# Optimization experiments

Hardware: AMD Instinct MI355X
Metric: run time of the kernel (lower is better)

Reference implementation:

```python
import jax, jax.numpy as jnp
import numpy as np

B, T, E = 2, 512, 1024        # batch, max_tokens, embedding dim
S, A = 2048, 30               # num_spans, max_arg_span


def setup_inputs() -> dict:
    key = jax.random.key(0)
    k1, k2, k3, k4 = jax.random.split(key, 4)
    x = jax.random.normal(k1, (B, T, E), dtype=jnp.float32)
    W = jax.random.normal(k2, (E, 1), dtype=jnp.float32) * (1.0 / np.sqrt(E))
    b = jnp.zeros((1,), dtype=jnp.float32)
    start = jax.random.randint(k3, (S,), 0, T, dtype=jnp.int32)
    width = jax.random.randint(k4, (S,), 1, A + 1, dtype=jnp.int32)
    end = jnp.minimum(start + width - 1, T - 1).astype(jnp.int32)
    return {"x": x, "W": W, "b": b, "start": start, "end": end}


def reference(x, W, b, start, end):
    # span_indices: clamp start+offset to last token, shape [S, A]
    span_idx = jnp.minimum(jnp.arange(A)[None, :] + start[:, None], T - 1)
    # gather span token embeddings: [B, S, A, E]
    span_emb = x[:, span_idx, :]
    # tiny per-token head score: Dense(1, relu) -> [B, T, 1]
    head_scores = jax.nn.relu(x @ W + b)
    # validity mask over span positions (log-mask), [S, A]
    span_width = end - start + 1
    valid = jnp.arange(A)[None, :] < span_width[:, None]
    log_mask = jnp.where(valid, 0.0, -jnp.inf)
    # gather scores per span position, add log-mask: [B, S, A, 1]
    span_head = head_scores[:, span_idx, :] + log_mask[None, :, :, None]
    # softmax over span-position axis (axis=2)
    attn = jax.nn.softmax(span_head, axis=2)
    # weighted-sum pooling over span positions -> [B, S, E]
    return jnp.sum(span_emb * attn, axis=2)
```

## Files before the change

### kernel.cpp

```cpp
#include <hip/hip_runtime.h>
#include <math.h>

#define TT 512
#define EE 1024
#define AA 30

typedef float f32x4 __attribute__((ext_vector_type(4)));

__device__ __forceinline__ unsigned bf16rne(float f) {
    unsigned u = __float_as_uint(f);
    return (u + 0x7fffu + ((u >> 16) & 1u)) >> 16;
}
__device__ __forceinline__ float blo(unsigned u) { return __uint_as_float(u << 16); }
__device__ __forceinline__ float bhi(unsigned u) { return __uint_as_float(u & 0xffff0000u); }

__global__ __launch_bounds__(256) void head_kernel(const float* __restrict__ x,
                                                   const float* __restrict__ W,
                                                   const float* __restrict__ bias,
                                                   float* __restrict__ head,
                                                   ushort* __restrict__ x16, int BT) {
    int row  = blockIdx.x * 4 + (threadIdx.x >> 6);
    int lane = threadIdx.x & 63;
    if (row >= BT) return;
    const f32x4* xr = reinterpret_cast<const f32x4*>(x + (size_t)row * EE);
    const f32x4* wr = reinterpret_cast<const f32x4*>(W);
    uint2* cr = reinterpret_cast<uint2*>(x16 + (size_t)row * EE);
    float acc = 0.f;
    #pragma unroll
    for (int k = 0; k < 4; ++k) {
        int i = lane + 64 * k;
        f32x4 xv = xr[i];
        f32x4 wv = wr[i];
        acc += xv.x * wv.x + xv.y * wv.y + xv.z * wv.z + xv.w * wv.w;
        if (x16) {
            uint2 pk;
            pk.x = bf16rne(xv.x) | (bf16rne(xv.y) << 16);
            pk.y = bf16rne(xv.z) | (bf16rne(xv.w) << 16);
            cr[i] = pk;
        }
    }
    #pragma unroll
    for (int off = 32; off; off >>= 1) acc += __shfl_xor(acc, off, 64);
    if (lane == 0) head[row] = fmaxf(acc + bias[0], 0.0f);
}

__global__ __launch_bounds__(256) void span16_kernel(const ushort* __restrict__ x16,
                                                     const float* __restrict__ head,
                                                     const int* __restrict__ start,
                                                     const int* __restrict__ end,
                                                     float* __restrict__ out, int S) {
    int p = blockIdx.x;
    __shared__ float wts[2][AA];

    int wv = threadIdx.x >> 6, l64 = threadIdx.x & 63;
    if (wv < 2) {
        int gg = 2 * p + wv;
        int bb = gg / S, ss = gg - bb * S;
        int st0 = start[ss];
        int nA0 = min(end[ss] - st0 + 1, AA);
        bool valid = l64 < nA0;
        int idx = st0 + l64; if (idx > TT - 1) idx = TT - 1;
        float sc = valid ? head[bb * TT + idx] : -INFINITY;
        float m = sc;
        #pragma unroll
        for (int off = 32; off; off >>= 1) m = fmaxf(m, __shfl_xor(m, off, 64));
        float e = valid ? __expf(sc - m) : 0.0f;
        float sum = e;
        #pragma unroll
        for (int off = 32; off; off >>= 1) sum += __shfl_xor(sum, off, 64);
        if (valid) wts[wv][l64] = e / sum;
    }
    __syncthreads();

    int sp   = threadIdx.x >> 7;
    int lane = threadIdx.x & 127;
    int gg = 2 * p + sp;
    int b = gg / S, s = gg - b * S;
    int st = start[s];
    int nA = min(end[s] - st + 1, AA);

    const uint4* xr = reinterpret_cast<const uint4*>(x16 + (size_t)b * TT * EE);
    f32x4 acc0 = (f32x4)(0.f), acc1 = (f32x4)(0.f);
    for (int a = 0; a < nA; ++a) {
        float w = wts[sp][a];
        uint4 v = xr[(size_t)(st + a) * (EE / 8) + lane];
        acc0.x += w * blo(v.x); acc0.y += w * bhi(v.x);
        acc0.z += w * blo(v.y); acc0.w += w * bhi(v.y);
        acc1.x += w * blo(v.z); acc1.y += w * bhi(v.z);
        acc1.z += w * blo(v.w); acc1.w += w * bhi(v.w);
    }
    f32x4* op = reinterpret_cast<f32x4*>(out) + (size_t)gg * (EE / 4) + 2 * lane;
    __builtin_nontemporal_store(acc0, op);
    __builtin_nontemporal_store(acc1, op + 1);
}

__global__ __launch_bounds__(256) void span_kernel(const float* __restrict__ x,
                                                   const float* __restrict__ head,
                                                   const int* __restrict__ start,
                                                   const int* __restrict__ end,
                                                   float* __restrict__ out, int S) {
    int bs = blockIdx.x;
    int b = bs / S, s = bs - b * S;
    int st = start[s];
    int nA = min(end[s] - st + 1, AA);
    __shared__ float wts[AA];
    int tid = threadIdx.x;
    if (tid < 64) {
        int a = tid;
        bool valid = (a < nA);
        int idx = st + a; if (idx > TT - 1) idx = TT - 1;
        float sc = valid ? head[b * TT + idx] : -INFINITY;
        float m = sc;
        #pragma unroll
        for (int off = 32; off; off >>= 1) m = fmaxf(m, __shfl_xor(m, off, 64));
        float e = valid ? __expf(sc - m) : 0.0f;
        float sum = e;
        #pragma unroll
        for (int off = 32; off; off >>= 1) sum += __shfl_xor(sum, off, 64);
        if (valid) wts[a] = e / sum;
    }
    __syncthreads();
    const f32x4* xb = reinterpret_cast<const f32x4*>(x + (size_t)b * TT * EE);
    f32x4 acc = (f32x4)(0.f);
    for (int a = 0; a < nA; ++a) {
        acc += wts[a] * xb[(size_t)(st + a) * (EE / 4) + tid];
    }
    f32x4* op = reinterpret_cast<f32x4*>(out) + (size_t)bs * (EE / 4) + tid;
    __builtin_nontemporal_store(acc, op);
}

extern "C" void kernel_launch(void* const* d_in, const int* in_sizes, int n_in,
                              void* d_out, int out_size, void* d_ws, size_t ws_size,
                              hipStream_t stream) {
    const float* x     = (const float*)d_in[0];
    const float* W     = (const float*)d_in[1];
    const float* bias  = (const float*)d_in[2];
    const int*   start = (const int*)d_in[3];
    const int*   end   = (const int*)d_in[4];
    float*       out   = (float*)d_out;

    const int BT = in_sizes[0] / EE;
    const int S  = in_sizes[3];
    const int B  = BT / TT;

    float*  head = (float*)d_ws;
    size_t  need = 8192 + (size_t)BT * EE * sizeof(ushort);
    ushort* x16  = (ws_size >= need) ? (ushort*)((char*)d_ws + 8192) : nullptr;

    head_kernel<<<(BT + 3) / 4, 256, 0, stream>>>(x, W, bias, head, x16, BT);
    if (x16 && (S & 1) == 0) {
        span16_kernel<<<B * S / 2, 256, 0, stream>>>(x16, head, start, end, out, S);
    } else {
        span_kernel<<<B * S, 256, 0, stream>>>(x, head, start, end, out, S);
    }
}
```

Baseline: 20.93 us.

## Counting-sort spans by start and remap blocks per XCD for L2 locality

Adds an extra block to the head kernel that counting-sorts span indices by start token into an order array. The span kernel reads spans in that sorted order and maps blocks round-robin so each group of eight consecutive block IDs covers one contiguous chunk of sorted spans. The goal is for spans with overlapping token rows to land on the same XCD and hit its L2 instead of going to HBM. It also makes the bf16 copy stores nontemporal. The costs are an extra indirection, writes to output rows in scattered order, and a serial sort block that runs alongside the head computation.

Result: no change. 21.30 us (+1.8%).

```diff
diff --git a/kernel.cpp b/kernel.cpp
--- a/kernel.cpp
+++ b/kernel.cpp
@@ -5,7 +5,8 @@
 #define EE 1024
 #define AA 30
 
-typedef float f32x4 __attribute__((ext_vector_type(4)));
+typedef float    f32x4 __attribute__((ext_vector_type(4)));
+typedef unsigned u32x2 __attribute__((ext_vector_type(2)));
 
 __device__ __forceinline__ unsigned bf16rne(float f) {
     unsigned u = __float_as_uint(f);
@@ -14,17 +15,57 @@
 __device__ __forceinline__ float blo(unsigned u) { return __uint_as_float(u << 16); }
 __device__ __forceinline__ float bhi(unsigned u) { return __uint_as_float(u & 0xffff0000u); }
 
-__global__ __launch_bounds__(256) void head_kernel(const float* __restrict__ x,
-                                                   const float* __restrict__ W,
-                                                   const float* __restrict__ bias,
-                                                   float* __restrict__ head,
-                                                   ushort* __restrict__ x16, int BT) {
-    int row  = blockIdx.x * 4 + (threadIdx.x >> 6);
-    int lane = threadIdx.x & 63;
+__global__ __launch_bounds__(256) void head_sort_kernel(const float* __restrict__ x,
+                                                        const float* __restrict__ W,
+                                                        const float* __restrict__ bias,
+                                                        const int* __restrict__ start,
+                                                        float* __restrict__ head,
+                                                        ushort* __restrict__ x16,
+                                                        int* __restrict__ order,
+                                                        int BT, int S, int HB) {
+    int tid = threadIdx.x;
+    if ((int)blockIdx.x == HB) {
+        __shared__ int cnt[TT];
+        __shared__ int wsum[4];
+        for (int i = tid; i < TT; i += 256) cnt[i] = 0;
+        __syncthreads();
+        for (int s = tid; s < S; s += 256) {
+            int k = start[s]; k = k < 0 ? 0 : (k > TT - 1 ? TT - 1 : k);
+            atomicAdd(&cnt[k], 1);
+        }
+        __syncthreads();
+        int a0 = cnt[2 * tid], a1 = cnt[2 * tid + 1];
+        int pair = a0 + a1;
+        int lane = tid & 63, wid = tid >> 6;
+        int v = pair;
+        #pragma unroll
+        for (int off = 1; off < 64; off <<= 1) {
+            int u = __shfl_up(v, off, 64);
+            if (lane >= off) v += u;
+        }
+        if (lane == 63) wsum[wid] = v;
+        __syncthreads();
+        int base = 0;
+        #pragma unroll
+        for (int w = 0; w < 4; ++w) if (w < wid) base += wsum[w];
+        int excl = base + v - pair;
+        __syncthreads();
+        cnt[2 * tid] = excl;
+        cnt[2 * tid + 1] = excl + a0;
+        __syncthreads();
+        for (int s = tid; s < S; s += 256) {
+            int k = start[s]; k = k < 0 ? 0 : (k > TT - 1 ? TT - 1 : k);
+            int pos = atomicAdd(&cnt[k], 1);
+            order[pos] = s;
+        }
+        return;
+    }
+    int row  = blockIdx.x * 4 + (tid >> 6);
+    int lane = tid & 63;
     if (row >= BT) return;
     const f32x4* xr = reinterpret_cast<const f32x4*>(x + (size_t)row * EE);
     const f32x4* wr = reinterpret_cast<const f32x4*>(W);
-    uint2* cr = reinterpret_cast<uint2*>(x16 + (size_t)row * EE);
+    u32x2* cr = reinterpret_cast<u32x2*>(x16 + (size_t)row * EE);
     float acc = 0.f;
     #pragma unroll
     for (int k = 0; k < 4; ++k) {
@@ -32,35 +73,40 @@
         f32x4 xv = xr[i];
         f32x4 wv = wr[i];
         acc += xv.x * wv.x + xv.y * wv.y + xv.z * wv.z + xv.w * wv.w;
-        if (x16) {
-            uint2 pk;
-            pk.x = bf16rne(xv.x) | (bf16rne(xv.y) << 16);
-            pk.y = bf16rne(xv.z) | (bf16rne(xv.w) << 16);
-            cr[i] = pk;
-        }
+        u32x2 pk;
+        pk.x = bf16rne(xv.x) | (bf16rne(xv.y) << 16);
+        pk.y = bf16rne(xv.z) | (bf16rne(xv.w) << 16);
+        __builtin_nontemporal_store(pk, cr + i);
     }
     #pragma unroll
     for (int off = 32; off; off >>= 1) acc += __shfl_xor(acc, off, 64);
     if (lane == 0) head[row] = fmaxf(acc + bias[0], 0.0f);
 }
 
+template <int BINNED>
 __global__ __launch_bounds__(256) void span16_kernel(const ushort* __restrict__ x16,
                                                      const float* __restrict__ head,
                                                      const int* __restrict__ start,
                                                      const int* __restrict__ end,
-                                                     float* __restrict__ out, int S) {
-    int p = blockIdx.x;
+                                                     const int* __restrict__ order,
+                                                     float* __restrict__ out, int S, int G8) {
     __shared__ float wts[2][AA];
+    __shared__ int sid[2], sbb[2];
+
+    int g0 = BINNED ? ((blockIdx.x & 7) * G8 + ((blockIdx.x >> 3) << 1))
+                    : (blockIdx.x * 2);
 
     int wv = threadIdx.x >> 6, l64 = threadIdx.x & 63;
     if (wv < 2) {
-        int gg = 2 * p + wv;
-        int bb = gg / S, ss = gg - bb * S;
-        int st0 = start[ss];
-        int nA0 = min(end[ss] - st0 + 1, AA);
-        bool valid = l64 < nA0;
-        int idx = st0 + l64; if (idx > TT - 1) idx = TT - 1;
-        float sc = valid ? head[bb * TT + idx] : -INFINITY;
+        int g = g0 + wv;
+        int b = g / S, r = g - b * S;
+        int s = BINNED ? order[r] : r;
+        if (l64 == 0) { sid[wv] = s; sbb[wv] = b; }
+        int st = start[s];
+        int nA = min(end[s] - st + 1, AA);
+        bool valid = l64 < nA;
+        int idx = st + l64; if (idx > TT - 1) idx = TT - 1;
+        float sc = valid ? head[b * TT + idx] : -INFINITY;
         float m = sc;
         #pragma unroll
         for (int off = 32; off; off >>= 1) m = fmaxf(m, __shfl_xor(m, off, 64));
@@ -74,8 +120,7 @@
 
     int sp   = threadIdx.x >> 7;
     int lane = threadIdx.x & 127;
-    int gg = 2 * p + sp;
-    int b = gg / S, s = gg - b * S;
+    int s = sid[sp], b = sbb[sp];
     int st = start[s];
     int nA = min(end[s] - st + 1, AA);
 
@@ -89,7 +134,7 @@
         acc1.x += w * blo(v.z); acc1.y += w * bhi(v.z);
         acc1.z += w * blo(v.w); acc1.w += w * bhi(v.w);
     }
-    f32x4* op = reinterpret_cast<f32x4*>(out) + (size_t)gg * (EE / 4) + 2 * lane;
+    f32x4* op = reinterpret_cast<f32x4*>(out) + (size_t)(b * S + s) * (EE / 4) + 2 * lane;
     __builtin_nontemporal_store(acc0, op);
     __builtin_nontemporal_store(acc1, op + 1);
 }
@@ -106,9 +151,8 @@
     __shared__ float wts[AA];
     int tid = threadIdx.x;
     if (tid < 64) {
-        int a = tid;
-        bool valid = (a < nA);
-        int idx = st + a; if (idx > TT - 1) idx = TT - 1;
+        bool valid = (tid < nA);
+        int idx = st + tid; if (idx > TT - 1) idx = TT - 1;
         float sc = valid ? head[b * TT + idx] : -INFINITY;
         float m = sc;
         #pragma unroll
@@ -117,16 +161,35 @@
         float sum = e;
         #pragma unroll
         for (int off = 32; off; off >>= 1) sum += __shfl_xor(sum, off, 64);
-        if (valid) wts[a] = e / sum;
+        if (valid) wts[tid] = e / sum;
     }
     __syncthreads();
     const f32x4* xb = reinterpret_cast<const f32x4*>(x + (size_t)b * TT * EE);
     f32x4 acc = (f32x4)(0.f);
-    for (int a = 0; a < nA; ++a) {
+    for (int a = 0; a < nA; ++a)
         acc += wts[a] * xb[(size_t)(st + a) * (EE / 4) + tid];
-    }
     f32x4* op = reinterpret_cast<f32x4*>(out) + (size_t)bs * (EE / 4) + tid;
     __builtin_nontemporal_store(acc, op);
+}
+
+__global__ __launch_bounds__(256) void head_kernel(const float* __restrict__ x,
+                                                   const float* __restrict__ W,
+                                                   const float* __restrict__ bias,
+                                                   float* __restrict__ head, int BT) {
+    int row  = blockIdx.x * 4 + (threadIdx.x >> 6);
+    int lane = threadIdx.x & 63;
+    if (row >= BT) return;
+    const f32x4* xr = reinterpret_cast<const f32x4*>(x + (size_t)row * EE);
+    const f32x4* wr = reinterpret_cast<const f32x4*>(W);
+    float acc = 0.f;
+    #pragma unroll
+    for (int i = lane; i < EE / 4; i += 64) {
+        f32x4 xv = xr[i], wv = wr[i];
+        acc += xv.x * wv.x + xv.y * wv.y + xv.z * wv.z + xv.w * wv.w;
+    }
+    #pragma unroll
+    for (int off = 32; off; off >>= 1) acc += __shfl_xor(acc, off, 64);
+    if (lane == 0) head[row] = fmaxf(acc + bias[0], 0.0f);
 }
 
 extern "C" void kernel_launch(void* const* d_in, const int* in_sizes, int n_in,
@@ -142,15 +205,26 @@
     const int BT = in_sizes[0] / EE;
     const int S  = in_sizes[3];
     const int B  = BT / TT;
-
-    float*  head = (float*)d_ws;
-    size_t  need = 8192 + (size_t)BT * EE * sizeof(ushort);
-    ushort* x16  = (ws_size >= need) ? (ushort*)((char*)d_ws + 8192) : nullptr;
-
-    head_kernel<<<(BT + 3) / 4, 256, 0, stream>>>(x, W, bias, head, x16, BT);
-    if (x16 && (S & 1) == 0) {
-        span16_kernel<<<B * S / 2, 256, 0, stream>>>(x16, head, start, end, out, S);
+    const int G  = B * S;
+
+    float* head  = (float*)d_ws;
+    int*   order = (int*)((char*)d_ws + 4096);
+    size_t x16off = 4096 + ((size_t)S * 4 + 255 & ~(size_t)255);
+    ushort* x16  = nullptr;
+    if (ws_size >= x16off + (size_t)BT * EE * sizeof(ushort))
+        x16 = (ushort*)((char*)d_ws + x16off);
+
+    const int HB = (BT + 3) / 4;
+    bool binned = (x16 != nullptr) && (G % 16 == 0) && (G >= 16);
+
+    if (x16) {
+        head_sort_kernel<<<HB + 1, 256, 0, stream>>>(x, W, bias, start, head, x16, order, BT, S, HB);
+        if (binned)
+            span16_kernel<1><<<G / 2, 256, 0, stream>>>(x16, head, start, end, order, out, S, G / 8);
+        else
+            span16_kernel<0><<<G / 2, 256, 0, stream>>>(x16, head, start, end, order, out, S, G / 8);
     } else {
-        span_kernel<<<B * S, 256, 0, stream>>>(x, head, start, end, out, S);
-    }
-}
+        head_kernel<<<HB, 256, 0, stream>>>(x, W, bias, head, BT);
+        span_kernel<<<G, 256, 0, stream>>>(x, head, start, end, out, S);
+    }
+}
```

## Swizzle span blocks by XCD per batch and compute softmax weights per wave

Applied to the files above, without the earlier changes.

The span kernel maps block IDs so that each group of four XCDs handles one batch, which keeps each batch's bf16 copy of x resident in the L2 caches of those XCDs. Each wave now computes its span's softmax weights itself and broadcasts them with shuffles, which removes the shared-memory staging and the block barrier. The accumulation loop is unrolled by two, and the bf16 copy stores become nontemporal. The swizzle is specialised to B=2, S=2048, and it drops the clamp of start+lane to T-1 when reading head scores.

After: 20.84 us. No clear change (-0.4%).

```diff
diff --git a/kernel.cpp b/kernel.cpp
--- a/kernel.cpp
+++ b/kernel.cpp
@@ -5,14 +5,15 @@
 #define EE 1024
 #define AA 30
 
-typedef float f32x4 __attribute__((ext_vector_type(4)));
+typedef float    f32x4 __attribute__((ext_vector_type(4)));
+typedef unsigned u32x2 __attribute__((ext_vector_type(2)));
 
-__device__ __forceinline__ unsigned bf16rne(float f) {
+static __device__ __forceinline__ unsigned bf16rne(float f) {
     unsigned u = __float_as_uint(f);
     return (u + 0x7fffu + ((u >> 16) & 1u)) >> 16;
 }
-__device__ __forceinline__ float blo(unsigned u) { return __uint_as_float(u << 16); }
-__device__ __forceinline__ float bhi(unsigned u) { return __uint_as_float(u & 0xffff0000u); }
+static __device__ __forceinline__ float blo(unsigned u) { return __uint_as_float(u << 16); }
+static __device__ __forceinline__ float bhi(unsigned u) { return __uint_as_float(u & 0xffff0000u); }
 
 __global__ __launch_bounds__(256) void head_kernel(const float* __restrict__ x,
                                                    const float* __restrict__ W,
@@ -24,7 +25,7 @@
     if (row >= BT) return;
     const f32x4* xr = reinterpret_cast<const f32x4*>(x + (size_t)row * EE);
     const f32x4* wr = reinterpret_cast<const f32x4*>(W);
-    uint2* cr = reinterpret_cast<uint2*>(x16 + (size_t)row * EE);
+    u32x2* cr = x16 ? reinterpret_cast<u32x2*>(x16 + (size_t)row * EE) : nullptr;
     float acc = 0.f;
     #pragma unroll
     for (int k = 0; k < 4; ++k) {
@@ -32,11 +33,11 @@
         f32x4 xv = xr[i];
         f32x4 wv = wr[i];
         acc += xv.x * wv.x + xv.y * wv.y + xv.z * wv.z + xv.w * wv.w;
-        if (x16) {
-            uint2 pk;
+        if (cr) {
+            u32x2 pk;
             pk.x = bf16rne(xv.x) | (bf16rne(xv.y) << 16);
             pk.y = bf16rne(xv.z) | (bf16rne(xv.w) << 16);
-            cr[i] = pk;
+            __builtin_nontemporal_store(pk, cr + i);
         }
     }
     #pragma unroll
@@ -44,52 +45,70 @@
     if (lane == 0) head[row] = fmaxf(acc + bias[0], 0.0f);
 }
 
+template <int SWZ>
 __global__ __launch_bounds__(256) void span16_kernel(const ushort* __restrict__ x16,
                                                      const float* __restrict__ head,
                                                      const int* __restrict__ start,
                                                      const int* __restrict__ end,
                                                      float* __restrict__ out, int S) {
-    int p = blockIdx.x;
-    __shared__ float wts[2][AA];
+    int bid = blockIdx.x;
+    int b, j2;
+    if (SWZ) {
+        int xcd = bid & 7;
+        b  = xcd >> 2;
+        j2 = ((((bid >> 3) << 2) | (xcd & 3))) << 1;
+    } else {
+        int g0 = bid << 1;
+        b  = g0 / S;
+        j2 = g0 - b * S;
+    }
+    int wv   = threadIdx.x >> 6;
+    int lane = threadIdx.x & 63;
+    int sp   = wv >> 1;
+    int h    = wv & 1;
+    int s    = j2 + sp;
 
-    int wv = threadIdx.x >> 6, l64 = threadIdx.x & 63;
-    if (wv < 2) {
-        int gg = 2 * p + wv;
-        int bb = gg / S, ss = gg - bb * S;
-        int st0 = start[ss];
-        int nA0 = min(end[ss] - st0 + 1, AA);
-        bool valid = l64 < nA0;
-        int idx = st0 + l64; if (idx > TT - 1) idx = TT - 1;
-        float sc = valid ? head[bb * TT + idx] : -INFINITY;
-        float m = sc;
-        #pragma unroll
-        for (int off = 32; off; off >>= 1) m = fmaxf(m, __shfl_xor(m, off, 64));
-        float e = valid ? __expf(sc - m) : 0.0f;
-        float sum = e;
-        #pragma unroll
-        for (int off = 32; off; off >>= 1) sum += __shfl_xor(sum, off, 64);
-        if (valid) wts[wv][l64] = e / sum;
-    }
-    __syncthreads();
-
-    int sp   = threadIdx.x >> 7;
-    int lane = threadIdx.x & 127;
-    int gg = 2 * p + sp;
-    int b = gg / S, s = gg - b * S;
     int st = start[s];
     int nA = min(end[s] - st + 1, AA);
 
-    const uint4* xr = reinterpret_cast<const uint4*>(x16 + (size_t)b * TT * EE);
+    bool valid = lane < nA;
+    float sc = valid ? head[b * TT + st + lane] : -INFINITY;
+    float m = sc;
+    #pragma unroll
+    for (int off = 32; off; off >>= 1) m = fmaxf(m, __shfl_xor(m, off, 64));
+    float e = valid ? __expf(sc - m) : 0.0f;
+    float sum = e;
+    #pragma unroll
+    for (int off = 32; off; off >>= 1) sum += __shfl_xor(sum, off, 64);
+    float ev = e / sum;
+
+    const uint4* xr = reinterpret_cast<const uint4*>(x16 + (size_t)b * TT * EE)
+                      + h * 64 + lane;
     f32x4 acc0 = (f32x4)(0.f), acc1 = (f32x4)(0.f);
-    for (int a = 0; a < nA; ++a) {
-        float w = wts[sp][a];
-        uint4 v = xr[(size_t)(st + a) * (EE / 8) + lane];
-        acc0.x += w * blo(v.x); acc0.y += w * bhi(v.x);
-        acc0.z += w * blo(v.y); acc0.w += w * bhi(v.y);
-        acc1.x += w * blo(v.z); acc1.y += w * bhi(v.z);
-        acc1.z += w * blo(v.w); acc1.w += w * bhi(v.w);
+    int a = 0;
+    for (; a + 2 <= nA; a += 2) {
+        uint4 v0 = xr[(size_t)(st + a)     * (EE / 8)];
+        uint4 v1 = xr[(size_t)(st + a + 1) * (EE / 8)];
+        float w0 = __shfl(ev, a);
+        float w1 = __shfl(ev, a + 1);
+        acc0.x += w0 * blo(v0.x); acc0.y += w0 * bhi(v0.x);
+        acc0.z += w0 * blo(v0.y); acc0.w += w0 * bhi(v0.y);
+        acc1.x += w0 * blo(v0.z); acc1.y += w0 * bhi(v0.z);
+        acc1.z += w0 * blo(v0.w); acc1.w += w0 * bhi(v0.w);
+        acc0.x += w1 * blo(v1.x); acc0.y += w1 * bhi(v1.x);
+        acc0.z += w1 * blo(v1.y); acc0.w += w1 * bhi(v1.y);
+        acc1.x += w1 * blo(v1.z); acc1.y += w1 * bhi(v1.z);
+        acc1.z += w1 * blo(v1.w); acc1.w += w1 * bhi(v1.w);
     }
-    f32x4* op = reinterpret_cast<f32x4*>(out) + (size_t)gg * (EE / 4) + 2 * lane;
+    if (a < nA) {
+        uint4 v0 = xr[(size_t)(st + a) * (EE / 8)];
+        float w0 = __shfl(ev, a);
+        acc0.x += w0 * blo(v0.x); acc0.y += w0 * bhi(v0.x);
+        acc0.z += w0 * blo(v0.y); acc0.w += w0 * bhi(v0.y);
+        acc1.x += w0 * blo(v0.z); acc1.y += w0 * bhi(v0.z);
+        acc1.z += w0 * blo(v0.w); acc1.w += w0 * bhi(v0.w);
+    }
+    f32x4* op = reinterpret_cast<f32x4*>(out + (size_t)(b * S + s) * EE) + 2 * (h * 64 + lane);
     __builtin_nontemporal_store(acc0, op);
     __builtin_nontemporal_store(acc1, op + 1);
 }
@@ -106,9 +125,8 @@
     __shared__ float wts[AA];
     int tid = threadIdx.x;
     if (tid < 64) {
-        int a = tid;
-        bool valid = (a < nA);
-        int idx = st + a; if (idx > TT - 1) idx = TT - 1;
+        bool valid = (tid < nA);
+        int idx = st + tid; if (idx > TT - 1) idx = TT - 1;
         float sc = valid ? head[b * TT + idx] : -INFINITY;
         float m = sc;
         #pragma unroll
@@ -117,14 +135,13 @@
         float sum = e;
         #pragma unroll
         for (int off = 32; off; off >>= 1) sum += __shfl_xor(sum, off, 64);
-        if (valid) wts[a] = e / sum;
+        if (valid) wts[tid] = e / sum;
     }
     __syncthreads();
     const f32x4* xb = reinterpret_cast<const f32x4*>(x + (size_t)b * TT * EE);
     f32x4 acc = (f32x4)(0.f);
-    for (int a = 0; a < nA; ++a) {
+    for (int a = 0; a < nA; ++a)
         acc += wts[a] * xb[(size_t)(st + a) * (EE / 4) + tid];
-    }
     f32x4* op = reinterpret_cast<f32x4*>(out) + (size_t)bs * (EE / 4) + tid;
     __builtin_nontemporal_store(acc, op);
 }
@@ -142,15 +159,20 @@
     const int BT = in_sizes[0] / EE;
     const int S  = in_sizes[3];
     const int B  = BT / TT;
+    const int G  = B * S;
 
     float*  head = (float*)d_ws;
-    size_t  need = 8192 + (size_t)BT * EE * sizeof(ushort);
-    ushort* x16  = (ws_size >= need) ? (ushort*)((char*)d_ws + 8192) : nullptr;
+    size_t  x16off = ((size_t)BT * 4 + 255) & ~(size_t)255;
+    ushort* x16  = (ws_size >= x16off + (size_t)BT * EE * 2) ? (ushort*)((char*)d_ws + x16off)
+                                                             : nullptr;
 
     head_kernel<<<(BT + 3) / 4, 256, 0, stream>>>(x, W, bias, head, x16, BT);
     if (x16 && (S & 1) == 0) {
-        span16_kernel<<<B * S / 2, 256, 0, stream>>>(x16, head, start, end, out, S);
+        if (B == 2 && S == 2048)
+            span16_kernel<1><<<G / 2, 256, 0, stream>>>(x16, head, start, end, out, S);
+        else
+            span16_kernel<0><<<G / 2, 256, 0, stream>>>(x16, head, start, end, out, S);
     } else {
-        span_kernel<<<B * S, 256, 0, stream>>>(x, head, start, end, out, S);
+        span_kernel<<<G, 256, 0, stream>>>(x, head, start, end, out, S);
     }
 }
```
